# Kernel optimization log

Measured on AMD Instinct MI355X. Metric: run time of the kernel, lower is better.

The kernel has to match this reference:

```python
import jax, jax.numpy as jnp
import numpy as np

N_SEG = 1024  # segments per image (ids are contiguous in [0, N_SEG) after reindex_batch_segments)


def setup_inputs() -> dict:
    key = jax.random.key(0)
    k1, k2, k3, k4 = jax.random.split(key, 4)
    B, C, Hf, Wf = 4, 256, 16, 16
    H, W = 512, 512
    F_out = 192
    features = jax.random.normal(k1, (B, C, Hf, Wf), dtype=jnp.float32)
    w_conv = jax.random.normal(k2, (F_out, C), dtype=jnp.float32) / np.sqrt(C)
    b_conv = jax.random.normal(k3, (F_out,), dtype=jnp.float32) * 0.01
    segment = jax.random.randint(k4, (B, H, W), 0, N_SEG, dtype=jnp.int32)
    return {"features": features, "w_conv": w_conv, "b_conv": b_conv, "segment": segment}


def reference(features, w_conv, b_conv, segment):
    # features: (B, C, Hf, Wf) backbone output; segment: (B, H, W) int ids in [0, N_SEG)
    B, C, Hf, Wf = features.shape
    _, H, W = segment.shape
    # F.interpolate(..., mode='bilinear', align_corners=False) == half-pixel linear resize
    up = jax.image.resize(features, (B, C, H, W), method="bilinear")
    pix = up.transpose(0, 2, 3, 1).reshape(B * H * W, C)  # (B*H*W, C)
    # offset per-image segment ids into a global id space: id + b * N_SEG
    seg = (segment.reshape(B, H * W) + (jnp.arange(B, dtype=segment.dtype) * N_SEG)[:, None]).reshape(-1)
    sums = jax.ops.segment_sum(pix, seg, num_segments=B * N_SEG)              # (B*N, C)
    cnt = jax.ops.segment_sum(jnp.ones((B * H * W,), pix.dtype), seg, num_segments=B * N_SEG)
    mean = sums / jnp.maximum(cnt, 1.0)[:, None]
    feats = mean.reshape(B, N_SEG, C)                                          # (B, N, C)
    # last_conv: 1x1 Conv1d (C -> F_out) applied on (B, C, N), then permute(0, 2, 1)
    out = jnp.einsum("bnc,fc->bnf", feats, w_conv) + b_conv                    # (B, N, F_out)
    return out, segment
```

## Files before the change

### kernel.cpp

```cpp
#include <hip/hip_runtime.h>
#include <hip/hip_bf16.h>

constexpr int B_   = 4;
constexpr int C_   = 256;
constexpr int HF   = 16;
constexpr int WF   = 16;
constexpr int HH   = 512;
constexpr int WW   = 512;
constexpr int NSEG = 1024;
constexpr int FOUT = 192;
constexpr int NCELL = HF * WF;
constexpr int QCB   = 256;
constexpr int GPB   = 48;

__device__ void gemm_P_body(int gp, const float* __restrict__ feat,
                            const float* __restrict__ w, float* __restrict__ P) {
    int b  = gp / 12;
    int f0 = (gp % 12) * 16;
    int ij = threadIdx.x;
    const float* Fb = feat + (size_t)b * C_ * NCELL + ij;

    float acc[16] = {};
    for (int c0 = 0; c0 < C_; c0 += 4) {
        float fv0 = Fb[(size_t)(c0 + 0) * NCELL];
        float fv1 = Fb[(size_t)(c0 + 1) * NCELL];
        float fv2 = Fb[(size_t)(c0 + 2) * NCELL];
        float fv3 = Fb[(size_t)(c0 + 3) * NCELL];
        #pragma unroll
        for (int j = 0; j < 16; ++j) {
            float4 wv = *reinterpret_cast<const float4*>(&w[(size_t)(f0 + j) * C_ + c0]);
            acc[j] += fv0 * wv.x + fv1 * wv.y + fv2 * wv.z + fv3 * wv.w;
        }
    }
    float* Pp = P + (size_t)b * NCELL * FOUT + (size_t)ij * FOUT + f0;
    #pragma unroll
    for (int j4 = 0; j4 < 4; ++j4)
        *reinterpret_cast<float4*>(Pp + j4 * 4) =
            make_float4(acc[j4 * 4 + 0], acc[j4 * 4 + 1], acc[j4 * 4 + 2], acc[j4 * 4 + 3]);
}

__device__ __forceinline__ unsigned tapw(int v, int cc) {
    if (v < 0 || v >= 512) return 0u;
    int twov = 2 * v - 31;
    int num  = ((twov % 64) + 64) % 64;
    int iv   = (twov - num) >> 6;
    int v0 = max(iv, 0), v1 = min(iv + 1, 15);
    return (unsigned)((v0 == cc ? 64 - num : 0) + (v1 == cc ? num : 0));
}

struct CS { unsigned lbin[NSEG]; unsigned wc[64]; };

__device__ void quad_cell_body(int qb, const int* __restrict__ seg,
                               float* __restrict__ segout, float* __restrict__ AT,
                               CS& sm) {
    int tid   = threadIdx.x;
    int b     = qb >> 6;
    int cell0 = (qb & 63) * 4;
    int cy  = cell0 >> 4, cx0 = cell0 & 15;
    int ys  = 32 * cy - 16;

    int r  = tid >> 2;
    int y  = ys + r;
    unsigned wrv = tapw(y, cy);
    int yc = min(max(y, 0), HH - 1);
    int cg = (tid & 3) * 16;
    const int* srow = seg + (size_t)b * (HH * WW) + (size_t)yc * WW;

    #pragma unroll
    for (int i = 0; i < 4; ++i) {
        int cell = cell0 + i;
        int cx   = cx0 + i;
        int xs   = 32 * cx - 16;
        int cb   = (b << 8) | cell;

        const int4* sv = reinterpret_cast<const int4*>(seg + (size_t)cb * 1024);
        float4*     ov = reinterpret_cast<float4*>(segout + (size_t)cb * 1024);
        int4 pv = sv[tid];

        #pragma unroll
        for (int j = 0; j < 4; ++j) sm.lbin[tid * 4 + j] = 0u;
        if (tid < 64) sm.wc[tid] = tapw(xs + tid, cx);

        int x0 = xs + cg;
        int xc = min(max(x0, 0), WW - 16);
        const int4* lrow = reinterpret_cast<const int4*>(srow + xc);
        int4 v0 = lrow[0], v1 = lrow[1], v2 = lrow[2], v3 = lrow[3];

        ov[tid] = make_float4((float)pv.x, (float)pv.y, (float)pv.z, (float)pv.w);
        __syncthreads();

        uint4 wa  = *reinterpret_cast<const uint4*>(&sm.wc[cg + 0]);
        uint4 wb  = *reinterpret_cast<const uint4*>(&sm.wc[cg + 4]);
        uint4 wcv = *reinterpret_cast<const uint4*>(&sm.wc[cg + 8]);
        uint4 wd  = *reinterpret_cast<const uint4*>(&sm.wc[cg + 12]);

        atomicAdd(&sm.lbin[v0.x], wrv * wa.x);
        atomicAdd(&sm.lbin[v0.y], wrv * wa.y);
        atomicAdd(&sm.lbin[v0.z], wrv * wa.z);
        atomicAdd(&sm.lbin[v0.w], wrv * wa.w);
        atomicAdd(&sm.lbin[v1.x], wrv * wb.x);
        atomicAdd(&sm.lbin[v1.y], wrv * wb.y);
        atomicAdd(&sm.lbin[v1.z], wrv * wb.z);
        atomicAdd(&sm.lbin[v1.w], wrv * wb.w);
        atomicAdd(&sm.lbin[v2.x], wrv * wcv.x);
        atomicAdd(&sm.lbin[v2.y], wrv * wcv.y);
        atomicAdd(&sm.lbin[v2.z], wrv * wcv.z);
        atomicAdd(&sm.lbin[v2.w], wrv * wcv.w);
        atomicAdd(&sm.lbin[v3.x], wrv * wd.x);
        atomicAdd(&sm.lbin[v3.y], wrv * wd.y);
        atomicAdd(&sm.lbin[v3.z], wrv * wd.z);
        atomicAdd(&sm.lbin[v3.w], wrv * wd.w);
        __syncthreads();

        float4* dst = reinterpret_cast<float4*>(AT + ((size_t)(b * NCELL + cell)) * NSEG);
        constexpr float SCL = 1.0f / 4096.0f;
        dst[tid] = make_float4(sm.lbin[tid * 4 + 0] * SCL, sm.lbin[tid * 4 + 1] * SCL,
                               sm.lbin[tid * 4 + 2] * SCL, sm.lbin[tid * 4 + 3] * SCL);
        __syncthreads();
    }
}

__global__ __launch_bounds__(256) void k_phase1(const int* __restrict__ seg,
                                                float* __restrict__ segout,
                                                float* __restrict__ AT,
                                                const float* __restrict__ feat,
                                                const float* __restrict__ w,
                                                float* __restrict__ P) {
    __shared__ CS sm;
    int blk = blockIdx.x;
    if (blk < GPB) gemm_P_body(blk, feat, w, P);
    else           quad_cell_body(blk - GPB, seg, segout, AT, sm);
}

__global__ __launch_bounds__(256) void k_gemm_out(const float* __restrict__ AT,
                                                  const float* __restrict__ P,
                                                  const float* __restrict__ bias,
                                                  float* __restrict__ out) {
    int ft = blockIdx.x % 3;
    int st = blockIdx.x / 3;
    int b  = st >> 5;
    int s0 = (st & 31) * 32;

    const float* ATb = AT + (size_t)b * NCELL * NSEG;
    const float* Pb  = P  + (size_t)b * NCELL * FOUT;

    __shared__ float As[32][33];
    __shared__ float Ps[32][65];

    int tid = threadIdx.x;
    int tx = tid & 15, ty = tid >> 4;
    float acc[2][4] = {};
    float cnt[2] = {};

    for (int k0 = 0; k0 < NCELL; k0 += 32) {
        {
            int kk = tid >> 3, e4 = (tid & 7) * 4;
            float4 va = *reinterpret_cast<const float4*>(&ATb[(size_t)(k0 + kk) * NSEG + s0 + e4]);
            As[kk][e4 + 0] = va.x; As[kk][e4 + 1] = va.y;
            As[kk][e4 + 2] = va.z; As[kk][e4 + 3] = va.w;
            #pragma unroll
            for (int l = 0; l < 2; ++l) {
                int li = tid * 2 + l;
                int kp = li >> 4, e = (li & 15) * 4;
                float4 vp = *reinterpret_cast<const float4*>(&Pb[(size_t)(k0 + kp) * FOUT + ft * 64 + e]);
                Ps[kp][e + 0] = vp.x; Ps[kp][e + 1] = vp.y;
                Ps[kp][e + 2] = vp.z; Ps[kp][e + 3] = vp.w;
            }
        }
        __syncthreads();
        #pragma unroll
        for (int kk = 0; kk < 32; ++kk) {
            float ar[2], wr[4];
            #pragma unroll
            for (int i = 0; i < 2; ++i) { ar[i] = As[kk][ty * 2 + i]; cnt[i] += ar[i]; }
            #pragma unroll
            for (int j = 0; j < 4; ++j) wr[j] = Ps[kk][tx * 4 + j];
            #pragma unroll
            for (int i = 0; i < 2; ++i)
                #pragma unroll
                for (int j = 0; j < 4; ++j) acc[i][j] += ar[i] * wr[j];
        }
        __syncthreads();
    }

    #pragma unroll
    for (int i = 0; i < 2; ++i) {
        int row = b * NSEG + s0 + ty * 2 + i;
        float rinv = 1.0f / fmaxf(cnt[i], 1.0f);
        #pragma unroll
        for (int j = 0; j < 4; ++j) {
            int f = ft * 64 + tx * 4 + j;
            out[(size_t)row * FOUT + f] = acc[i][j] * rinv + bias[f];
        }
    }
}

extern "C" void kernel_launch(void* const* d_in, const int* in_sizes, int n_in,
                              void* d_out, int out_size, void* d_ws, size_t ws_size,
                              hipStream_t stream) {
    const float* feat = (const float*)d_in[0];
    const float* w    = (const float*)d_in[1];
    const float* bias = (const float*)d_in[2];
    const int*   seg  = (const int*)d_in[3];

    float* out    = (float*)d_out;
    float* segout = out + (size_t)B_ * NSEG * FOUT;

    char* wsb = (char*)d_ws;
    float* AT = (float*)wsb;
    float* P  = (float*)(wsb + (5u << 20));

    k_phase1  <<<GPB + QCB, 256, 0, stream>>>(seg, segout, AT, feat, w, P);
    k_gemm_out<<<(B_ * NSEG / 32) * (FOUT / 64), 256, 0, stream>>>(AT, P, bias, out);
}
```

Before: 59.42 us.

## Process four cells concurrently per 1024-thread block instead of sequential quad loop

```diff
diff --git a/kernel.cpp b/kernel.cpp
--- a/kernel.cpp
+++ b/kernel.cpp
@@ -10,14 +10,22 @@
 constexpr int NSEG = 1024;
 constexpr int FOUT = 192;
 constexpr int NCELL = HF * WF;
-constexpr int QCB   = 256;
-constexpr int GPB   = 48;
-
-__device__ void gemm_P_body(int gp, const float* __restrict__ feat,
+constexpr int QC    = 256;
+constexpr int QP    = 12;
+
+__device__ __forceinline__ unsigned tapw(int v, int cc) {
+    if (v < 0 || v >= 512) return 0u;
+    int twov = 2 * v - 31;
+    int num  = ((twov % 64) + 64) % 64;
+    int iv   = (twov - num) >> 6;
+    int v0 = max(iv, 0), v1 = min(iv + 1, 15);
+    return (unsigned)((v0 == cc ? 64 - num : 0) + (v1 == cc ? num : 0));
+}
+
+__device__ void gemm_P_body(int gp, int ij, const float* __restrict__ feat,
                             const float* __restrict__ w, float* __restrict__ P) {
     int b  = gp / 12;
     int f0 = (gp % 12) * 16;
-    int ij = threadIdx.x;
     const float* Fb = feat + (size_t)b * C_ * NCELL + ij;
 
     float acc[16] = {};
@@ -39,97 +47,82 @@
             make_float4(acc[j4 * 4 + 0], acc[j4 * 4 + 1], acc[j4 * 4 + 2], acc[j4 * 4 + 3]);
 }
 
-__device__ __forceinline__ unsigned tapw(int v, int cc) {
-    if (v < 0 || v >= 512) return 0u;
-    int twov = 2 * v - 31;
-    int num  = ((twov % 64) + 64) % 64;
-    int iv   = (twov - num) >> 6;
-    int v0 = max(iv, 0), v1 = min(iv + 1, 15);
-    return (unsigned)((v0 == cc ? 64 - num : 0) + (v1 == cc ? num : 0));
-}
-
-struct CS { unsigned lbin[NSEG]; unsigned wc[64]; };
-
-__device__ void quad_cell_body(int qb, const int* __restrict__ seg,
-                               float* __restrict__ segout, float* __restrict__ AT,
-                               CS& sm) {
-    int tid   = threadIdx.x;
-    int b     = qb >> 6;
-    int cell0 = (qb & 63) * 4;
-    int cy  = cell0 >> 4, cx0 = cell0 & 15;
-    int ys  = 32 * cy - 16;
-
-    int r  = tid >> 2;
+__device__ void cell_body(int cb, int stid, const int* __restrict__ seg,
+                          float* __restrict__ segout, float* __restrict__ AT,
+                          unsigned* __restrict__ lbin, unsigned* __restrict__ wc) {
+    int b    = cb >> 8;
+    int cell = cb & 255;
+    int cy = cell >> 4, cx = cell & 15;
+    int ys = 32 * cy - 16, xs = 32 * cx - 16;
+
+    const int4* sv = reinterpret_cast<const int4*>(seg + (size_t)cb * 1024);
+    float4*     ov = reinterpret_cast<float4*>(segout + (size_t)cb * 1024);
+    int4 pv = sv[stid];
+
+    #pragma unroll
+    for (int j = 0; j < 4; ++j) lbin[stid * 4 + j] = 0u;
+    if (stid < 64) wc[stid] = tapw(xs + stid, cx);
+
+    int r  = stid >> 2;
     int y  = ys + r;
     unsigned wrv = tapw(y, cy);
     int yc = min(max(y, 0), HH - 1);
-    int cg = (tid & 3) * 16;
-    const int* srow = seg + (size_t)b * (HH * WW) + (size_t)yc * WW;
-
-    #pragma unroll
-    for (int i = 0; i < 4; ++i) {
-        int cell = cell0 + i;
-        int cx   = cx0 + i;
-        int xs   = 32 * cx - 16;
-        int cb   = (b << 8) | cell;
-
-        const int4* sv = reinterpret_cast<const int4*>(seg + (size_t)cb * 1024);
-        float4*     ov = reinterpret_cast<float4*>(segout + (size_t)cb * 1024);
-        int4 pv = sv[tid];
-
-        #pragma unroll
-        for (int j = 0; j < 4; ++j) sm.lbin[tid * 4 + j] = 0u;
-        if (tid < 64) sm.wc[tid] = tapw(xs + tid, cx);
-
-        int x0 = xs + cg;
-        int xc = min(max(x0, 0), WW - 16);
-        const int4* lrow = reinterpret_cast<const int4*>(srow + xc);
-        int4 v0 = lrow[0], v1 = lrow[1], v2 = lrow[2], v3 = lrow[3];
-
-        ov[tid] = make_float4((float)pv.x, (float)pv.y, (float)pv.z, (float)pv.w);
-        __syncthreads();
-
-        uint4 wa  = *reinterpret_cast<const uint4*>(&sm.wc[cg + 0]);
-        uint4 wb  = *reinterpret_cast<const uint4*>(&sm.wc[cg + 4]);
-        uint4 wcv = *reinterpret_cast<const uint4*>(&sm.wc[cg + 8]);
-        uint4 wd  = *reinterpret_cast<const uint4*>(&sm.wc[cg + 12]);
-
-        atomicAdd(&sm.lbin[v0.x], wrv * wa.x);
-        atomicAdd(&sm.lbin[v0.y], wrv * wa.y);
-        atomicAdd(&sm.lbin[v0.z], wrv * wa.z);
-        atomicAdd(&sm.lbin[v0.w], wrv * wa.w);
-        atomicAdd(&sm.lbin[v1.x], wrv * wb.x);
-        atomicAdd(&sm.lbin[v1.y], wrv * wb.y);
-        atomicAdd(&sm.lbin[v1.z], wrv * wb.z);
-        atomicAdd(&sm.lbin[v1.w], wrv * wb.w);
-        atomicAdd(&sm.lbin[v2.x], wrv * wcv.x);
-        atomicAdd(&sm.lbin[v2.y], wrv * wcv.y);
-        atomicAdd(&sm.lbin[v2.z], wrv * wcv.z);
-        atomicAdd(&sm.lbin[v2.w], wrv * wcv.w);
-        atomicAdd(&sm.lbin[v3.x], wrv * wd.x);
-        atomicAdd(&sm.lbin[v3.y], wrv * wd.y);
-        atomicAdd(&sm.lbin[v3.z], wrv * wd.z);
-        atomicAdd(&sm.lbin[v3.w], wrv * wd.w);
-        __syncthreads();
-
-        float4* dst = reinterpret_cast<float4*>(AT + ((size_t)(b * NCELL + cell)) * NSEG);
-        constexpr float SCL = 1.0f / 4096.0f;
-        dst[tid] = make_float4(sm.lbin[tid * 4 + 0] * SCL, sm.lbin[tid * 4 + 1] * SCL,
-                               sm.lbin[tid * 4 + 2] * SCL, sm.lbin[tid * 4 + 3] * SCL);
-        __syncthreads();
-    }
-}
-
-__global__ __launch_bounds__(256) void k_phase1(const int* __restrict__ seg,
-                                                float* __restrict__ segout,
-                                                float* __restrict__ AT,
-                                                const float* __restrict__ feat,
-                                                const float* __restrict__ w,
-                                                float* __restrict__ P) {
-    __shared__ CS sm;
+    int cg = (stid & 3) * 16;
+    int x0 = xs + cg;
+    int xc = min(max(x0, 0), WW - 16);
+
+    const int4* lrow = reinterpret_cast<const int4*>(seg + (size_t)b * (HH * WW) + (size_t)yc * WW + xc);
+    int4 v0 = lrow[0], v1 = lrow[1], v2 = lrow[2], v3 = lrow[3];
+
+    ov[stid] = make_float4((float)pv.x, (float)pv.y, (float)pv.z, (float)pv.w);
+    __syncthreads();
+
+    uint4 wa  = *reinterpret_cast<const uint4*>(&wc[cg + 0]);
+    uint4 wb  = *reinterpret_cast<const uint4*>(&wc[cg + 4]);
+    uint4 wcv = *reinterpret_cast<const uint4*>(&wc[cg + 8]);
+    uint4 wd  = *reinterpret_cast<const uint4*>(&wc[cg + 12]);
+
+    atomicAdd(&lbin[v0.x], wrv * wa.x);
+    atomicAdd(&lbin[v0.y], wrv * wa.y);
+    atomicAdd(&lbin[v0.z], wrv * wa.z);
+    atomicAdd(&lbin[v0.w], wrv * wa.w);
+    atomicAdd(&lbin[v1.x], wrv * wb.x);
+    atomicAdd(&lbin[v1.y], wrv * wb.y);
+    atomicAdd(&lbin[v1.z], wrv * wb.z);
+    atomicAdd(&lbin[v1.w], wrv * wb.w);
+    atomicAdd(&lbin[v2.x], wrv * wcv.x);
+    atomicAdd(&lbin[v2.y], wrv * wcv.y);
+    atomicAdd(&lbin[v2.z], wrv * wcv.z);
+    atomicAdd(&lbin[v2.w], wrv * wcv.w);
+    atomicAdd(&lbin[v3.x], wrv * wd.x);
+    atomicAdd(&lbin[v3.y], wrv * wd.y);
+    atomicAdd(&lbin[v3.z], wrv * wd.z);
+    atomicAdd(&lbin[v3.w], wrv * wd.w);
+    __syncthreads();
+
+    float4* dst = reinterpret_cast<float4*>(AT + ((size_t)(b * NCELL + cell)) * NSEG);
+    constexpr float SCL = 1.0f / 4096.0f;
+    dst[stid] = make_float4(lbin[stid * 4 + 0] * SCL, lbin[stid * 4 + 1] * SCL,
+                            lbin[stid * 4 + 2] * SCL, lbin[stid * 4 + 3] * SCL);
+}
+
+__global__ __launch_bounds__(1024) void k_phase1(const int* __restrict__ seg,
+                                                 float* __restrict__ segout,
+                                                 float* __restrict__ AT,
+                                                 const float* __restrict__ feat,
+                                                 const float* __restrict__ w,
+                                                 float* __restrict__ P) {
+    __shared__ unsigned lbin[4][NSEG];
+    __shared__ unsigned wc[4][64];
     int blk = blockIdx.x;
-    if (blk < GPB) gemm_P_body(blk, feat, w, P);
-    else           quad_cell_body(blk - GPB, seg, segout, AT, sm);
+    int tid = threadIdx.x;
+    int sub = tid >> 8, stid = tid & 255;
+
+    if (blk >= QC) {
+        gemm_P_body(((blk - QC) << 2) | sub, stid, feat, w, P);
+        return;
+    }
+    cell_body((blk << 2) | sub, stid, seg, segout, AT, lbin[sub], wc[sub]);
 }
 
 __global__ __launch_bounds__(256) void k_gemm_out(const float* __restrict__ AT,
@@ -210,6 +203,6 @@
     float* AT = (float*)wsb;
     float* P  = (float*)(wsb + (5u << 20));
 
-    k_phase1  <<<GPB + QCB, 256, 0, stream>>>(seg, segout, AT, feat, w, P);
+    k_phase1  <<<QC + QP, 1024, 0, stream>>>(seg, segout, AT, feat, w, P);
     k_gemm_out<<<(B_ * NSEG / 32) * (FOUT / 64), 256, 0, stream>>>(AT, P, bias, out);
 }
```

Result: slower. 156.4 us (+163.1%).
